# Optimization experiments

Measured on AMD Instinct MI355X. Metric: run time of the kernel, lower is better.

## Reference

```python
import jax, jax.numpy as jnp
import numpy as np

B, S, D, A = 16, 2048, 512, 512

def setup_inputs() -> dict:
    key = jax.random.key(0)
    ks = jax.random.split(key, 7)
    scale = 1.0 / np.sqrt(D)
    return {
        "query": jax.random.normal(ks[0], (B, S, D), dtype=jnp.float32),
        "key_": jax.random.normal(ks[1], (B, S, D), dtype=jnp.float32),
        "value": jax.random.normal(ks[2], (B, S, D), dtype=jnp.float32),
        "Wq": jax.random.normal(ks[3], (D, A), dtype=jnp.float32) * scale,
        "Wk": jax.random.normal(ks[4], (D, A), dtype=jnp.float32) * scale,
        "Wv": jax.random.normal(ks[5], (D, A), dtype=jnp.float32) * scale,
        "Ws": jax.random.normal(ks[6], (A, 1), dtype=jnp.float32) * (1.0 / np.sqrt(A)),
    }

def reference(query, key_, value, Wq, Wk, Wv, Ws):
    # Dense projections (no bias): [B,S,D] @ [D,A] -> [B,S,A]
    q = jnp.einsum("bsd,da->bsa", query, Wq)
    k = jnp.einsum("bsd,da->bsa", key_, Wk)
    v = jnp.einsum("bsd,da->bsa", value, Wv)
    # Additive (Bahdanau) scores: tanh(q+k) @ Ws -> [B,S]
    scores = jnp.einsum("bsa,a->bs", jnp.tanh(q + k), Ws[:, 0])
    attention_weights = jax.nn.softmax(scores, axis=1)[..., None]  # [B,S,1]
    context_vector = jnp.sum(attention_weights * v, axis=1)        # [B,A]
    return context_vector, attention_weights
```

## Files before the change

### kernel.cpp

```cpp
#include <hip/hip_runtime.h>
#include <stdint.h>

#define B_ 16
#define S_ 2048
#define D_ 512
#define A_ 512
#define M_TOT (B_ * S_)

typedef __attribute__((ext_vector_type(4))) float f32x4;
typedef __attribute__((ext_vector_type(8))) short bf16x8;

__device__ inline unsigned short f2bf(float f) {
  union { float f; unsigned int u; } c; c.f = f;
  unsigned int u = c.u;
  unsigned int r = (u + 0x7fffu + ((u >> 16) & 1u)) >> 16;
  return (unsigned short)r;
}

__device__ inline float fast_tanh(float x) {
  float e = __expf(2.0f * x);
  return 1.0f - 2.0f * __builtin_amdgcn_rcpf(e + 1.0f);
}

__device__ inline void gload_lds16(const void* g, void* l) {
  __builtin_amdgcn_global_load_lds((const __attribute__((address_space(1))) void*)g,
                                   (__attribute__((address_space(3))) void*)l, 16, 0, 0);
}

__global__ __launch_bounds__(256) void k0_pack_w(const float* __restrict__ Wq,
                                                 const float* __restrict__ Wk,
                                                 unsigned short* __restrict__ WT) {
  __shared__ unsigned short tile[64][65];
  int bid = blockIdx.x;
  int dt = bid & 15, at = bid >> 4;
  int d0 = dt * 64, a0 = at * 64;
  int t = threadIdx.x;
  int col = t & 63, rbase = t >> 6;
#pragma unroll
  for (int r8 = 0; r8 < 16; ++r8) {
    int row = r8 * 4 + rbase;
    int dcat = d0 + row;
    float f = (dcat < 512) ? Wq[(size_t)dcat * 512 + a0 + col]
                           : Wk[(size_t)(dcat - 512) * 512 + a0 + col];
    tile[row][col] = f2bf(f);
  }
  __syncthreads();
#pragma unroll
  for (int r8 = 0; r8 < 16; ++r8) {
    int arow = r8 * 4 + rbase;
    WT[(size_t)(a0 + arow) * 1024 + d0 + col] = tile[col][arow];
  }
}

__global__ __launch_bounds__(512, 4) void k1_scores(
    const float* __restrict__ Q, const float* __restrict__ K,
    const unsigned short* __restrict__ WT, const float* __restrict__ Wsv,
    float* __restrict__ score) {
  __shared__ unsigned short Al[2][64 * 32];
  __shared__ unsigned short Bl[2][512 * 32];
  __shared__ float sws[512];
  __shared__ float scw[8][64];

  const int t = threadIdx.x;
  const int lane = t & 63, w = t >> 6;
  const int frow = lane & 15, fsl = lane >> 4;
  const int row0 = (int)blockIdx.x * 64;

  sws[t] = Wsv[t];

  const int ar = t >> 3, ak = (t & 7) * 4;
  const int wchunk = (t & 7) >> 1;
  const int wbyte = ar * 64 + ((wchunk ^ ((ar >> 1) & 3)) * 16) + (t & 1) * 8;

  float4 areg[2];

  auto issueA = [&](int kt, int j) {
    int kcat = kt * 32;
    const float* src = (kcat < 512) ? Q : K;
    areg[j] = *(const float4*)(src + (size_t)(row0 + ar) * 512 + (kcat & 511) + ak);
  };
  auto stageAW = [&](int j) {
    float4 f = areg[j];
    uint2 d;
    d.x = f2bf(f.x) | ((unsigned)f2bf(f.y) << 16);
    d.y = f2bf(f.z) | ((unsigned)f2bf(f.w) << 16);
    *(uint2*)((char*)&Al[j][0] + wbyte) = d;
  };
  auto stageB = [&](int kt) {
    int j = kt & 1;
    int kb = kt * 64;
#pragma unroll
    for (int q = 0; q < 4; ++q) {
      int p = (w * 4 + q) * 64 + lane;
      int row = p >> 2;
      int sl = (p & 3) ^ ((row >> 1) & 3);
      const char* g = (const char*)WT + (size_t)row * 2048 + kb + sl * 16;
      char* l = (char*)&Bl[j][0] + (size_t)(w * 4 + q) * 1024;
      gload_lds16(g, l);
    }
  };

  f32x4 acc[4][4];
#pragma unroll
  for (int m = 0; m < 4; ++m)
#pragma unroll
    for (int n = 0; n < 4; ++n) acc[m][n] = (f32x4){0.f, 0.f, 0.f, 0.f};

  issueA(0, 0);
  stageAW(0);
  stageB(0);
  issueA(1, 1);

#pragma unroll 2
  for (int kt = 0; kt < 32; ++kt) {
    const int cur = kt & 1;
    __syncthreads();
    if (kt + 2 < 32) issueA(kt + 2, cur);
    if (kt + 1 < 32) { stageAW(cur ^ 1); stageB(kt + 1); }
    bf16x8 af[4], bfr[4];
    const int ch = (fsl ^ ((frow >> 1) & 3)) * 16;
#pragma unroll
    for (int m = 0; m < 4; ++m)
      af[m] = *(const bf16x8*)((const char*)&Al[cur][0] + (m * 16 + frow) * 64 + ch);
#pragma unroll
    for (int n = 0; n < 4; ++n)
      bfr[n] = *(const bf16x8*)((const char*)&Bl[cur][0] + (w * 64 + n * 16 + frow) * 64 + ch);
#pragma unroll
    for (int m = 0; m < 4; ++m)
#pragma unroll
      for (int n = 0; n < 4; ++n)
        acc[m][n] = __builtin_amdgcn_mfma_f32_16x16x32_bf16(af[m], bfr[n], acc[m][n], 0, 0, 0);
  }

#pragma unroll
  for (int m = 0; m < 4; ++m) {
#pragma unroll
    for (int ii = 0; ii < 4; ++ii) {
      float s = 0.f;
#pragma unroll
      for (int n = 0; n < 4; ++n)
        s += fast_tanh(acc[m][n][ii]) * sws[w * 64 + n * 16 + frow];
      s += __shfl_xor(s, 1);
      s += __shfl_xor(s, 2);
      s += __shfl_xor(s, 4);
      s += __shfl_xor(s, 8);
      if (frow == 0) scw[w][m * 16 + fsl * 4 + ii] = s;
    }
  }
  __syncthreads();
  if (t < 64) {
    float s = 0.f;
#pragma unroll
    for (int ww = 0; ww < 8; ++ww) s += scw[ww][t];
    score[row0 + t] = s;
  }
}

__global__ __launch_bounds__(256) void k2_softmax(const float* __restrict__ score,
                                                  float* __restrict__ outw) {
  int b = blockIdx.x, t = threadIdx.x;
  int lane = t & 63, wave = t >> 6;
  __shared__ float red[4], red2[4];
  float v[8];
  float mx = -1e30f;
#pragma unroll
  for (int e = 0; e < 8; ++e) {
    float p = score[(size_t)b * S_ + e * 256 + t];
    v[e] = p;
    mx = fmaxf(mx, p);
  }
  for (int off = 1; off < 64; off <<= 1) mx = fmaxf(mx, __shfl_xor(mx, off));
  if (lane == 0) red[wave] = mx;
  __syncthreads();
  mx = fmaxf(fmaxf(red[0], red[1]), fmaxf(red[2], red[3]));
  float sum = 0.f;
#pragma unroll
  for (int e = 0; e < 8; ++e) { v[e] = expf(v[e] - mx); sum += v[e]; }
  for (int off = 1; off < 64; off <<= 1) sum += __shfl_xor(sum, off);
  if (lane == 0) red2[wave] = sum;
  __syncthreads();
  sum = red2[0] + red2[1] + red2[2] + red2[3];
  float inv = 1.f / sum;
#pragma unroll
  for (int e = 0; e < 8; ++e)
    outw[(size_t)b * S_ + e * 256 + t] = v[e] * inv;
}

__global__ __launch_bounds__(256) void k3_vsum(const float* __restrict__ value,
                                               const float* __restrict__ w,
                                               float* __restrict__ upart) {
  int bid = blockIdx.x;
  int dh = bid & 1, sc = (bid >> 1) & 15, b = bid >> 5;
  int t = threadIdx.x;
  int dg = t & 63, sg = t >> 6;
  __shared__ float wl[128];
  __shared__ f32x4 red[4][64];
  int s0 = sc * 128;
  if (t < 128) wl[t] = w[(size_t)b * S_ + s0 + t];
  __syncthreads();
  const float* vp = value + ((size_t)b * S_ + s0) * 512 + dh * 256 + dg * 4;
  f32x4 a = (f32x4){0.f, 0.f, 0.f, 0.f};
  for (int s = sg; s < 128; s += 4) {
    float4 v4 = *(const float4*)(vp + (size_t)s * 512);
    float ws = wl[s];
    a[0] += ws * v4.x; a[1] += ws * v4.y; a[2] += ws * v4.z; a[3] += ws * v4.w;
  }
  red[sg][dg] = a;
  __syncthreads();
  if (sg == 0) {
    f32x4 r = red[0][dg] + red[1][dg] + red[2][dg] + red[3][dg];
    float* dst = upart + (size_t)(sc * 16 + b) * 512 + dh * 256 + dg * 4;
    dst[0] = r[0]; dst[1] = r[1]; dst[2] = r[2]; dst[3] = r[3];
  }
}

__global__ __launch_bounds__(512) void k4_ctx(const float* __restrict__ upart,
                                              const float* __restrict__ Wv,
                                              float* __restrict__ out) {
  int b = blockIdx.x, t = threadIdx.x;
  __shared__ float ul[512];
  float u = 0.f;
#pragma unroll
  for (int c = 0; c < 16; ++c) u += upart[(size_t)(c * 16 + b) * 512 + t];
  ul[t] = u;
  __syncthreads();
  float acc = 0.f;
#pragma unroll 8
  for (int d = 0; d < 512; ++d) acc += ul[d] * Wv[(size_t)d * 512 + t];
  out[(size_t)b * 512 + t] = acc;
}

extern "C" void kernel_launch(void* const* d_in, const int* in_sizes, int n_in,
                              void* d_out, int out_size, void* d_ws, size_t ws_size,
                              hipStream_t stream) {
  const float* Q  = (const float*)d_in[0];
  const float* Kk = (const float*)d_in[1];
  const float* V  = (const float*)d_in[2];
  const float* Wq = (const float*)d_in[3];
  const float* Wk = (const float*)d_in[4];
  const float* Wv = (const float*)d_in[5];
  const float* Ws = (const float*)d_in[6];
  float* out = (float*)d_out;

  char* ws = (char*)d_ws;
  unsigned short* WT = (unsigned short*)ws;
  float* score = (float*)(ws + (1 << 20));
  float* upart = (float*)(ws + (1 << 20) + (512 << 10));

  float* outw = out + B_ * A_;

  k0_pack_w<<<dim3(128), dim3(256), 0, stream>>>(Wq, Wk, WT);
  k1_scores<<<dim3(512), dim3(512), 0, stream>>>(Q, Kk, WT, Ws, score);
  k2_softmax<<<dim3(16), dim3(256), 0, stream>>>(score, outw);
  k3_vsum<<<dim3(512), dim3(256), 0, stream>>>(V, outw, upart);
  k4_ctx<<<dim3(16), dim3(512), 0, stream>>>(upart, Wv, out);
}
```

Measured before the change: 101.5 us.

## Double score GEMM row tile to 128 and hand-pipeline loads with explicit waitcnt

The scores GEMM block now covers 128 rows instead of 64, so each B tile of the packed weights loaded into LDS feeds twice as many MFMAs, and the grid halves to 256 blocks. The main loop is restructured into explicit ping-pong phases. Each phase issues the global loads two steps ahead, uses targeted s_waitcnt plus raw s_barrier instead of __syncthreads, and raises wave priority around the MFMA block. The Ws vector goes to registers and the reduction scratch reuses the A buffer in LDS. The trade-off is double the accumulator registers, occupancy bounded at 2 blocks per CU, and only 256 blocks for the whole GPU.

```diff
diff --git a/kernel.cpp b/kernel.cpp
--- a/kernel.cpp
+++ b/kernel.cpp
@@ -5,7 +5,6 @@
 #define S_ 2048
 #define D_ 512
 #define A_ 512
-#define M_TOT (B_ * S_)
 
 typedef __attribute__((ext_vector_type(4))) float f32x4;
 typedef __attribute__((ext_vector_type(8))) short bf16x8;
@@ -52,106 +51,128 @@
   }
 }
 
-__global__ __launch_bounds__(512, 4) void k1_scores(
+__global__ __launch_bounds__(512, 2) void k1_scores(
     const float* __restrict__ Q, const float* __restrict__ K,
     const unsigned short* __restrict__ WT, const float* __restrict__ Wsv,
     float* __restrict__ score) {
-  __shared__ unsigned short Al[2][64 * 32];
+  __shared__ unsigned short Al[2][128 * 32];
   __shared__ unsigned short Bl[2][512 * 32];
-  __shared__ float sws[512];
-  __shared__ float scw[8][64];
 
   const int t = threadIdx.x;
   const int lane = t & 63, w = t >> 6;
   const int frow = lane & 15, fsl = lane >> 4;
-  const int row0 = (int)blockIdx.x * 64;
-
-  sws[t] = Wsv[t];
-
-  const int ar = t >> 3, ak = (t & 7) * 4;
-  const int wchunk = (t & 7) >> 1;
-  const int wbyte = ar * 64 + ((wchunk ^ ((ar >> 1) & 3)) * 16) + (t & 1) * 8;
-
-  float4 areg[2];
-
-  auto issueA = [&](int kt, int j) {
-    int kcat = kt * 32;
-    const float* src = (kcat < 512) ? Q : K;
-    areg[j] = *(const float4*)(src + (size_t)(row0 + ar) * 512 + (kcat & 511) + ak);
-  };
-  auto stageAW = [&](int j) {
-    float4 f = areg[j];
-    uint2 d;
-    d.x = f2bf(f.x) | ((unsigned)f2bf(f.y) << 16);
-    d.y = f2bf(f.z) | ((unsigned)f2bf(f.w) << 16);
-    *(uint2*)((char*)&Al[j][0] + wbyte) = d;
-  };
-  auto stageB = [&](int kt) {
-    int j = kt & 1;
-    int kb = kt * 64;
+  const int row0 = (int)blockIdx.x * 128;
+
+  const int ar = t >> 2, ak = (t & 3) * 8;
+  const int abyte = ar * 64 + (((t & 3) ^ ((ar >> 1) & 3)) * 16);
+
+  float4 rA0[2], rA1[2];
+
+  auto issueA = [&](int p, float4* r) {
+    const float* src = (p < 16) ? Q : K;
+    const float* ap = src + (size_t)(row0 + ar) * 512 + ((p * 32) & 511) + ak;
+    r[0] = *(const float4*)(ap);
+    r[1] = *(const float4*)(ap + 4);
+  };
+  auto writeA = [&](const float4* r, int buf) {
+    uint4 d;
+    d.x = f2bf(r[0].x) | ((unsigned)f2bf(r[0].y) << 16);
+    d.y = f2bf(r[0].z) | ((unsigned)f2bf(r[0].w) << 16);
+    d.z = f2bf(r[1].x) | ((unsigned)f2bf(r[1].y) << 16);
+    d.w = f2bf(r[1].z) | ((unsigned)f2bf(r[1].w) << 16);
+    *(uint4*)((char*)&Al[buf][0] + abyte) = d;
+  };
+  auto stageB = [&](int p, int buf) {
 #pragma unroll
     for (int q = 0; q < 4; ++q) {
-      int p = (w * 4 + q) * 64 + lane;
-      int row = p >> 2;
-      int sl = (p & 3) ^ ((row >> 1) & 3);
-      const char* g = (const char*)WT + (size_t)row * 2048 + kb + sl * 16;
-      char* l = (char*)&Bl[j][0] + (size_t)(w * 4 + q) * 1024;
-      gload_lds16(g, l);
+      int pc = (w * 4 + q) * 64 + lane;
+      int row = pc >> 2;
+      int sl = (pc & 3) ^ ((row >> 1) & 3);
+      const char* g = (const char*)WT + (size_t)row * 2048 + p * 64 + sl * 16;
+      gload_lds16(g, (char*)&Bl[buf][0] + (size_t)(w * 4 + q) * 1024);
     }
   };
 
-  f32x4 acc[4][4];
-#pragma unroll
-  for (int m = 0; m < 4; ++m)
+  f32x4 acc[8][4];
+#pragma unroll
+  for (int m = 0; m < 8; ++m)
 #pragma unroll
     for (int n = 0; n < 4; ++n) acc[m][n] = (f32x4){0.f, 0.f, 0.f, 0.f};
 
-  issueA(0, 0);
-  stageAW(0);
-  stageB(0);
-  issueA(1, 1);
-
-#pragma unroll 2
-  for (int kt = 0; kt < 32; ++kt) {
-    const int cur = kt & 1;
-    __syncthreads();
-    if (kt + 2 < 32) issueA(kt + 2, cur);
-    if (kt + 1 < 32) { stageAW(cur ^ 1); stageB(kt + 1); }
-    bf16x8 af[4], bfr[4];
-    const int ch = (fsl ^ ((frow >> 1) & 3)) * 16;
-#pragma unroll
-    for (int m = 0; m < 4; ++m)
-      af[m] = *(const bf16x8*)((const char*)&Al[cur][0] + (m * 16 + frow) * 64 + ch);
+  const int ch = (fsl ^ ((frow >> 1) & 3)) * 16;
+
+  auto doMfma = [&](int CUR) {
+    bf16x8 af[8], bfr[4];
+#pragma unroll
+    for (int m = 0; m < 8; ++m)
+      af[m] = *(const bf16x8*)((const char*)&Al[CUR][0] + (m * 16 + frow) * 64 + ch);
 #pragma unroll
     for (int n = 0; n < 4; ++n)
-      bfr[n] = *(const bf16x8*)((const char*)&Bl[cur][0] + (w * 64 + n * 16 + frow) * 64 + ch);
-#pragma unroll
-    for (int m = 0; m < 4; ++m)
+      bfr[n] = *(const bf16x8*)((const char*)&Bl[CUR][0] + (w * 64 + n * 16 + frow) * 64 + ch);
+    __builtin_amdgcn_s_setprio(1);
+#pragma unroll
+    for (int m = 0; m < 8; ++m)
 #pragma unroll
       for (int n = 0; n < 4; ++n)
         acc[m][n] = __builtin_amdgcn_mfma_f32_16x16x32_bf16(af[m], bfr[n], acc[m][n], 0, 0, 0);
-  }
-
-#pragma unroll
-  for (int m = 0; m < 4; ++m) {
+    __builtin_amdgcn_s_setprio(0);
+  };
+
+  issueA(0, rA0);
+  stageB(0, 0);
+  __builtin_amdgcn_sched_barrier(0);
+  issueA(1, rA1);
+  writeA(rA0, 0);
+  asm volatile("s_waitcnt vmcnt(2) lgkmcnt(0)" ::: "memory");
+  __builtin_amdgcn_s_barrier();
+
+  auto phase = [&](int p, int CUR, float4* rCur, const float4* rNext) {
+    stageB(p + 1, CUR ^ 1);
+    __builtin_amdgcn_sched_barrier(0);
+    issueA(p + 2, rCur);
+    doMfma(CUR);
+    writeA(rNext, CUR ^ 1);
+    asm volatile("s_waitcnt vmcnt(2) lgkmcnt(0)" ::: "memory");
+    __builtin_amdgcn_s_barrier();
+  };
+
+  for (int kt2 = 0; kt2 < 15; ++kt2) {
+    phase(2 * kt2 + 0, 0, rA0, rA1);
+    phase(2 * kt2 + 1, 1, rA1, rA0);
+  }
+
+  stageB(31, 1);
+  doMfma(0);
+  writeA(rA1, 1);
+  asm volatile("s_waitcnt vmcnt(0) lgkmcnt(0)" ::: "memory");
+  __builtin_amdgcn_s_barrier();
+  doMfma(1);
+
+  float wsv[4];
+#pragma unroll
+  for (int n = 0; n < 4; ++n) wsv[n] = Wsv[w * 64 + n * 16 + frow];
+  __syncthreads();
+  float* scw = (float*)&Al[0][0];
+#pragma unroll
+  for (int m = 0; m < 8; ++m) {
 #pragma unroll
     for (int ii = 0; ii < 4; ++ii) {
       float s = 0.f;
 #pragma unroll
       for (int n = 0; n < 4; ++n)
-        s += fast_tanh(acc[m][n][ii]) * sws[w * 64 + n * 16 + frow];
+        s += fast_tanh(acc[m][n][ii]) * wsv[n];
       s += __shfl_xor(s, 1);
       s += __shfl_xor(s, 2);
       s += __shfl_xor(s, 4);
       s += __shfl_xor(s, 8);
-      if (frow == 0) scw[w][m * 16 + fsl * 4 + ii] = s;
+      if (frow == 0) scw[w * 128 + m * 16 + fsl * 4 + ii] = s;
     }
   }
   __syncthreads();
-  if (t < 64) {
+  if (t < 128) {
     float s = 0.f;
 #pragma unroll
-    for (int ww = 0; ww < 8; ++ww) s += scw[ww][t];
+    for (int ww = 0; ww < 8; ++ww) s += scw[ww * 128 + t];
     score[row0 + t] = s;
   }
 }
@@ -250,7 +271,7 @@
   float* outw = out + B_ * A_;
 
   k0_pack_w<<<dim3(128), dim3(256), 0, stream>>>(Wq, Wk, WT);
-  k1_scores<<<dim3(512), dim3(512), 0, stream>>>(Q, Kk, WT, Ws, score);
+  k1_scores<<<dim3(256), dim3(512), 0, stream>>>(Q, Kk, WT, Ws, score);
   k2_softmax<<<dim3(16), dim3(256), 0, stream>>>(score, outw);
   k3_vsum<<<dim3(512), dim3(256), 0, stream>>>(V, outw, upart);
   k4_ctx<<<dim3(16), dim3(512), 0, stream>>>(upart, Wv, out);
```

After: 97.07 us. 4.4% less time.
